# Performance work log

Hardware: AMD Instinct MI355X
Metric: run time of the kernel (lower is better)

Reference implementation:

```python
import jax, jax.numpy as jnp
import numpy as np

H = 16  # num_heads
EPS = 1e-6

def _sigma(t):
    # ELU(x)+1, the positive feature map used by Infini-attention linear memory
    return jax.nn.elu(t) + 1.0

def setup_inputs() -> dict:
    key = jax.random.key(0)
    ks = jax.random.split(key, 6)
    B, S, D = 1, 2048, 1024
    d = D // H
    std = 1.0 / np.sqrt(D)
    return {
        "x": jax.random.normal(ks[0], (B, S, D), dtype=jnp.float32),
        "M": jnp.zeros((H, d, d), dtype=jnp.float32),
        "z": jnp.zeros((H, d), dtype=jnp.float32),
        "Wq": jax.random.normal(ks[1], (D, D), dtype=jnp.float32) * std,
        "Wk": jax.random.normal(ks[2], (D, D), dtype=jnp.float32) * std,
        "Wv": jax.random.normal(ks[3], (D, D), dtype=jnp.float32) * std,
        "Wo": jax.random.normal(ks[4], (D, D), dtype=jnp.float32) * std,
        "beta": jnp.zeros((H,), dtype=jnp.float32),
    }

def reference(x, M, z, Wq, Wk, Wv, Wo, beta):
    B, S, D = x.shape
    d = D // H
    # projections -> [B, H, S, d]
    def proj(W):
        return (x @ W).reshape(B, S, H, d).transpose(0, 2, 1, 3)
    q, k, v = proj(Wq), proj(Wk), proj(Wv)

    # ---- local causal dot-product attention ----
    scale = 1.0 / jnp.sqrt(jnp.asarray(d, dtype=x.dtype))
    scores = jnp.einsum('bhqd,bhkd->bhqk', q, k) * scale  # [B,H,S,S]
    causal = jnp.tril(jnp.ones((S, S), dtype=bool))
    scores = jnp.where(causal, scores, jnp.asarray(-1e30, dtype=scores.dtype))
    A_dot = jnp.einsum('bhqk,bhkd->bhqd', jax.nn.softmax(scores, axis=-1), v)

    # ---- compressive memory retrieval (linear attention) ----
    sq = _sigma(q)                                       # [B,H,S,d]
    num = jnp.einsum('bhsd,hde->bhse', sq, M)            # [B,H,S,d]
    den = jnp.einsum('bhsd,hd->bhs', sq, z)[..., None]   # [B,H,S,1]
    A_mem = num / (den + EPS)

    # ---- learned gate blend ----
    g = jax.nn.sigmoid(beta).reshape(1, H, 1, 1)
    o = g * A_mem + (1.0 - g) * A_dot                    # [B,H,S,d]
    out = o.transpose(0, 2, 1, 3).reshape(B, S, D) @ Wo  # [B,S,D]

    # ---- memory update (stateful, no_grad in original) ----
    sk = _sigma(k)
    M_new = jax.lax.stop_gradient(M + jnp.einsum('bhsd,bhse->hde', sk, v))
    z_new = jax.lax.stop_gradient(z + sk.sum(axis=(0, 2)))
    return out, M_new, z_new
```

## Files before the change

kernel.cpp:

```cpp
#include <hip/hip_runtime.h>

#define S_LEN 2048
#define D_MODEL 1024
#define NH 16
#define DH 64

typedef __attribute__((ext_vector_type(8))) short bf16x8;
typedef __attribute__((ext_vector_type(4))) float f32x4;

__device__ __forceinline__ f32x4 mfma16(bf16x8 a, bf16x8 b, f32x4 c) {
  return __builtin_amdgcn_mfma_f32_16x16x32_bf16(a, b, c, 0, 0, 0);
}

__device__ __forceinline__ void ldst16(const ushort* g, ushort* l) {
  __builtin_amdgcn_global_load_lds(
      (const __attribute__((address_space(1))) void*)g,
      (__attribute__((address_space(3))) void*)l, 16, 0, 0);
}

__device__ __forceinline__ ushort bf16_rne(float f) {
  unsigned u = __float_as_uint(f);
  unsigned r = (u + 0x7FFFu + ((u >> 16) & 1u)) >> 16;
  return (ushort)r;
}
__device__ __forceinline__ float bf16_to_f(ushort u) {
  return __uint_as_float((unsigned)u << 16);
}

__global__ __launch_bounds__(256) void cast_bf16(
    const float* __restrict__ in, ushort* __restrict__ hi, int n4)
{
  int i = blockIdx.x * 256 + threadIdx.x;
  if (i >= n4) return;
  float4 v = ((const float4*)in)[i];
  ushort4 h;
  h.x = bf16_rne(v.x); h.y = bf16_rne(v.y);
  h.z = bf16_rne(v.z); h.w = bf16_rne(v.w);
  ((ushort4*)hi)[i] = h;
}

__global__ __launch_bounds__(256) void splitT(
    const float* __restrict__ W0, const float* __restrict__ W1,
    const float* __restrict__ W2, const float* __restrict__ W3,
    ushort* __restrict__ H0, ushort* __restrict__ L0,
    ushort* __restrict__ H1, ushort* __restrict__ L1,
    ushort* __restrict__ H2, ushort* __restrict__ L2,
    ushort* __restrict__ H3, ushort* __restrict__ L3)
{
  const int zz = blockIdx.z;
  const float* W = zz == 0 ? W0 : (zz == 1 ? W1 : (zz == 2 ? W2 : W3));
  ushort* H = zz == 0 ? H0 : (zz == 1 ? H1 : (zz == 2 ? H2 : H3));
  ushort* L = zz == 0 ? L0 : (zz == 1 ? L1 : (zz == 2 ? L2 : L3));
  __shared__ float ts[32][33];
  const int k0 = blockIdx.x * 32, n0 = blockIdx.y * 32;
  const int r = threadIdx.x >> 3, c4 = (threadIdx.x & 7) * 4;
  float4 v = *(const float4*)&W[(size_t)(k0 + r) * D_MODEL + n0 + c4];
  ts[r][c4 + 0] = v.x; ts[r][c4 + 1] = v.y; ts[r][c4 + 2] = v.z; ts[r][c4 + 3] = v.w;
  __syncthreads();
  ushort4 h, l;
#pragma unroll
  for (int ii = 0; ii < 4; ii++) {
    float f = ts[c4 + ii][r];
    ushort hb = bf16_rne(f);
    ushort lb = bf16_rne(f - __uint_as_float((unsigned)hb << 16));
    ((ushort*)&h)[ii] = hb;
    ((ushort*)&l)[ii] = lb;
  }
  *(ushort4*)&H[(size_t)(n0 + r) * D_MODEL + k0 + c4] = h;
  *(ushort4*)&L[(size_t)(n0 + r) * D_MODEL + k0 + c4] = l;
}

template<int TN>
__global__ __launch_bounds__(256, 3) void gemm_t(
    const ushort* __restrict__ Ah,
    const ushort* __restrict__ B0h, const ushort* __restrict__ B0l,
    const ushort* __restrict__ B1h, const ushort* __restrict__ B1l,
    const ushort* __restrict__ B2h, const ushort* __restrict__ B2l,
    float* __restrict__ C0, int K, int mode,
    ushort* __restrict__ aqb, ushort* __restrict__ akb,
    ushort* __restrict__ akbT, ushort* __restrict__ avbT)
{
  const int t = threadIdx.x;
  const int w = t >> 6, lane = t & 63;
  const int quad = lane >> 4, lr = lane & 15;
  const int bx = blockIdx.x;
  const int bw = (bx * TN) >> 10;
  const int n0 = (bx * TN) & 1023;
  const int m0 = blockIdx.y * 64;
  const ushort* Bh = bw == 0 ? B0h : (bw == 1 ? B1h : B2h);
  const ushort* Bl = bw == 0 ? B0l : (bw == 1 ? B1l : B2l);

  __shared__ ushort sAh[64 * 32], sBh[TN * 32], sBl[TN * 32];

  constexpr int NF = TN / 32;
  f32x4 acc[2][NF];
#pragma unroll
  for (int mi = 0; mi < 2; mi++)
#pragma unroll
    for (int ni = 0; ni < NF; ni++)
#pragma unroll
      for (int r = 0; r < 4; r++) acc[mi][ni][r] = 0.f;

  const int mbase = (w & 1) * 32;
  const int nbase = (w >> 1) * (TN / 2);
  const int rowA = w * 16 + (lane >> 2), kcA = (lane & 3) * 8;

  for (int k0 = 0; k0 < K; k0 += 32) {
    __syncthreads();
    ldst16(Ah + (size_t)(m0 + rowA) * K + k0 + kcA, &sAh[w * 512]);
#pragma unroll
    for (int i = 0; i < TN / 64; i++) {
      int rowB = w * (TN / 4) + i * 16 + (lane >> 2);
      int base = (w * (TN / 4) + i * 16) * 32;
      ldst16(Bh + (size_t)(n0 + rowB) * K + k0 + kcA, &sBh[base]);
      ldst16(Bl + (size_t)(n0 + rowB) * K + k0 + kcA, &sBl[base]);
    }
    __syncthreads();

    bf16x8 ah[2], bh[NF], bl[NF];
#pragma unroll
    for (int mi = 0; mi < 2; mi++)
      ah[mi] = *(const bf16x8*)&sAh[(mbase + mi * 16 + lr) * 32 + quad * 8];
#pragma unroll
    for (int ni = 0; ni < NF; ni++) {
      int rown = nbase + ni * 16 + lr;
      bh[ni] = *(const bf16x8*)&sBh[rown * 32 + quad * 8];
      bl[ni] = *(const bf16x8*)&sBl[rown * 32 + quad * 8];
    }
#pragma unroll
    for (int mi = 0; mi < 2; mi++)
#pragma unroll
      for (int ni = 0; ni < NF; ni++) {
        acc[mi][ni] = mfma16(ah[mi], bh[ni], acc[mi][ni]);
        acc[mi][ni] = mfma16(ah[mi], bl[ni], acc[mi][ni]);
      }
  }

  if (mode == 0) {
#pragma unroll
    for (int mi = 0; mi < 2; mi++)
#pragma unroll
      for (int ni = 0; ni < NF; ni++)
#pragma unroll
        for (int r = 0; r < 4; r++) {
          int row = m0 + mbase + mi * 16 + quad * 4 + r;
          int col = n0 + nbase + ni * 16 + lr;
          C0[(size_t)row * 1024 + col] = acc[mi][ni][r];
        }
  } else if (bw == 0) {
#pragma unroll
    for (int mi = 0; mi < 2; mi++)
#pragma unroll
      for (int ni = 0; ni < NF; ni++)
#pragma unroll
        for (int r = 0; r < 4; r++) {
          int row = m0 + mbase + mi * 16 + quad * 4 + r;
          int col = n0 + nbase + ni * 16 + lr;
          aqb[(size_t)row * 1024 + col] = bf16_rne(acc[mi][ni][r] * 0.125f);
        }
  } else if (bw == 1) {
#pragma unroll
    for (int mi = 0; mi < 2; mi++)
#pragma unroll
      for (int ni = 0; ni < NF; ni++) {
        int row0 = m0 + mbase + mi * 16 + quad * 4;
        int col = n0 + nbase + ni * 16 + lr;
        ushort4 pk;
#pragma unroll
        for (int r = 0; r < 4; r++) {
          ushort b = bf16_rne(acc[mi][ni][r]);
          ((ushort*)&pk)[r] = b;
          akb[(size_t)(row0 + r) * 1024 + col] = b;
        }
        *(ushort4*)&akbT[(size_t)col * 2048 + row0] = pk;
      }
  } else {
#pragma unroll
    for (int mi = 0; mi < 2; mi++)
#pragma unroll
      for (int ni = 0; ni < NF; ni++) {
        int row0 = m0 + mbase + mi * 16 + quad * 4;
        int col = n0 + nbase + ni * 16 + lr;
        ushort4 pk;
#pragma unroll
        for (int r = 0; r < 4; r++)
          ((ushort*)&pk)[r] = bf16_rne(acc[mi][ni][r]);
        *(ushort4*)&avbT[(size_t)col * 2048 + row0] = pk;
      }
  }
}

__global__ __launch_bounds__(256, 3) void attn_fused(
    const ushort* __restrict__ qb, const ushort* __restrict__ kb,
    const ushort* __restrict__ vbT, const ushort* __restrict__ kbT,
    const float* __restrict__ Mmem, const float* __restrict__ zmem,
    const float* __restrict__ beta,
    ushort* __restrict__ oh,
    float* __restrict__ Mout, float* __restrict__ zout)
{
  const int t = threadIdx.x;
  const int w = t >> 6, lane = t & 63;
  const int quad = lane >> 4, lr = lane & 15;

  __shared__ __align__(16) ushort sBuf[24576];
  __shared__ float drow[64];
  __shared__ float sL[64];

  if (blockIdx.x < 16) {
    const int h = blockIdx.x;
    float* red = (float*)sBuf;
    f32x4 acc[4][4];
#pragma unroll
    for (int mt = 0; mt < 4; mt++)
#pragma unroll
      for (int nt = 0; nt < 4; nt++)
#pragma unroll
        for (int r = 0; r < 4; r++) acc[mt][nt][r] = 0.f;
    float accZ[4] = {0.f, 0.f, 0.f, 0.f};

#pragma unroll 2
    for (int step = 0; step < 16; step++) {
      int k0 = w * 512 + step * 32;
      bf16x8 ah[4], al[4];
#pragma unroll
      for (int mt = 0; mt < 4; mt++) {
        bf16x8 raw = *(const bf16x8*)&kbT[(size_t)(h * 64 + mt * 16 + lr) * 2048 + k0 + quad * 8];
        bf16x8 hh, ll;
#pragma unroll
        for (int j = 0; j < 8; j++) {
          float f = bf16_to_f((ushort)raw[j]);
          float s = f > 0.f ? f + 1.f : __expf(f);
          accZ[mt] += s;
          ushort hb = bf16_rne(s);
          hh[j] = (short)hb;
          ll[j] = (short)bf16_rne(s - bf16_to_f(hb));
        }
        ah[mt] = hh; al[mt] = ll;
      }
      bf16x8 bv[4];
#pragma unroll
      for (int nt = 0; nt < 4; nt++)
        bv[nt] = *(const bf16x8*)&vbT[(size_t)(h * 64 + nt * 16 + lr) * 2048 + k0 + quad * 8];
#pragma unroll
      for (int mt = 0; mt < 4; mt++)
#pragma unroll
        for (int nt = 0; nt < 4; nt++) {
          acc[mt][nt] = mfma16(ah[mt], bv[nt], acc[mt][nt]);
          acc[mt][nt] = mfma16(al[mt], bv[nt], acc[mt][nt]);
        }
    }
#pragma unroll
    for (int mt = 0; mt < 4; mt++) {
      accZ[mt] += __shfl_xor(accZ[mt], 16);
      accZ[mt] += __shfl_xor(accZ[mt], 32);
    }
    if (w < 2) {
#pragma unroll
      for (int mt = 0; mt < 4; mt++)
#pragma unroll
        for (int nt = 0; nt < 4; nt++)
#pragma unroll
          for (int r = 0; r < 4; r++)
            red[w * 4096 + (mt * 16 + quad * 4 + r) * 64 + nt * 16 + lr] = acc[mt][nt][r];
    }
    __syncthreads();
    if (w >= 2) {
#pragma unroll
      for (int mt = 0; mt < 4; mt++)
#pragma unroll
        for (int nt = 0; nt < 4; nt++)
#pragma unroll
          for (int r = 0; r < 4; r++)
            red[(w - 2) * 4096 + (mt * 16 + quad * 4 + r) * 64 + nt * 16 + lr] += acc[mt][nt][r];
    }
    __syncthreads();
    for (int i = t; i < 4096; i += 256)
      Mout[(size_t)h * 4096 + i] = Mmem[(size_t)h * 4096 + i] + red[i] + red[4096 + i];
    __syncthreads();
    if (quad == 0) {
#pragma unroll
      for (int mt = 0; mt < 4; mt++)
        red[w * 64 + mt * 16 + lr] = accZ[mt];
    }
    __syncthreads();
    if (t < 64)
      zout[h * 64 + t] = zmem[h * 64 + t] + red[t] + red[64 + t] + red[128 + t] + red[192 + t];
    return;
  }

  const int a  = blockIdx.x - 16;
  const int h  = a >> 5;
  const int p  = (a >> 1) & 15;
  const int qt = (a & 1) ? p : 31 - p;
  const int s0 = qt * 64;
  const int ntiles = (qt + 2) >> 1;

  const int SPQ = 0, SK = 8192, SVT = 16384;

#pragma unroll
  for (int i = 0; i < 2; i++) {
    int li = w * 2 + i;
    int row = li * 8 + (lane >> 3);
    int cg = ((lane & 7) - row) & 7;
    ldst16(qb + (size_t)(s0 + row) * 1024 + h * 64 + cg * 8, &sBuf[SPQ + li * 512]);
  }
  __syncthreads();
  const int arow = w * 16 + lr;
  const bf16x8 aq0 = *(const bf16x8*)&sBuf[SPQ + arow * 64 + ((quad + arow) & 7) * 8];
  const bf16x8 aq1 = *(const bf16x8*)&sBuf[SPQ + arow * 64 + ((4 + quad + arow) & 7) * 8];

  f32x4 oacc[4];
#pragma unroll
  for (int ni = 0; ni < 4; ni++)
#pragma unroll
    for (int r = 0; r < 4; r++) oacc[ni][r] = 0.f;
  f32x4 lacc;
#pragma unroll
  for (int r = 0; r < 4; r++) lacc[r] = 0.f;
  bf16x8 bone;
#pragma unroll
  for (int j = 0; j < 8; j++) bone[j] = (lr == 0) ? (short)0x3F80 : (short)0;

  for (int jt = 0; jt < ntiles; jt++) {
    const int j0 = jt * 128;
    __syncthreads();
#pragma unroll
    for (int i = 0; i < 4; i++) {
      int li = w * 4 + i;
      int rowK = li * 8 + (lane >> 3);
      int cgK = ((lane & 7) - rowK) & 7;
      ldst16(kb + (size_t)(j0 + rowK) * 1024 + h * 64 + cgK * 8,
             &sBuf[SK + li * 512]);
      int rowV = li * 4 + (lane >> 4);
      int cgV = ((lane & 15) - rowV) & 15;
      ldst16(vbT + (size_t)(h * 64 + rowV) * 2048 + j0 + cgV * 8,
             &sBuf[SVT + li * 512]);
    }
    __syncthreads();

    f32x4 sc[8];
#pragma unroll
    for (int nj = 0; nj < 8; nj++) {
      int brow = nj * 16 + lr;
      bf16x8 b0 = *(const bf16x8*)&sBuf[SK + brow * 64 + ((quad + brow) & 7) * 8];
      bf16x8 b1 = *(const bf16x8*)&sBuf[SK + brow * 64 + ((4 + quad + brow) & 7) * 8];
      f32x4 z4; z4[0] = z4[1] = z4[2] = z4[3] = 0.f;
      z4 = mfma16(aq0, b0, z4);
      sc[nj] = mfma16(aq1, b1, z4);
    }
    if (jt == ntiles - 1) {
#pragma unroll
      for (int nj = 0; nj < 8; nj++)
#pragma unroll
        for (int r = 0; r < 4; r++)
          if (j0 + nj * 16 + lr > s0 + w * 16 + quad * 4 + r) sc[nj][r] = -1e30f;
    }

#pragma unroll
    for (int nj = 0; nj < 8; nj++)
#pragma unroll
      for (int r = 0; r < 4; r++) {
        float e = exp2f(fmaf(sc[nj][r], 1.4426950408889634f, -23.083120654223414f));
        int rr2 = w * 16 + quad * 4 + r;
        sBuf[SPQ + rr2 * 128 + ((nj * 16 + lr + rr2 * 8) & 127)] = bf16_rne(e);
      }

    bf16x8 ap[4];
#pragma unroll
    for (int kf = 0; kf < 4; kf++)
      ap[kf] = *(const bf16x8*)&sBuf[SPQ + arow * 128 + ((kf * 32 + quad * 8 + arow * 8) & 127)];
#pragma unroll
    for (int ni = 0; ni < 4; ni++) {
      int brow = ni * 16 + lr;
#pragma unroll
      for (int kf = 0; kf < 4; kf++) {
        bf16x8 bv = *(const bf16x8*)&sBuf[SVT + brow * 128 + ((kf * 32 + quad * 8 + brow * 8) & 127)];
        oacc[ni] = mfma16(ap[kf], bv, oacc[ni]);
      }
    }
#pragma unroll
    for (int kf = 0; kf < 4; kf++)
      lacc = mfma16(ap[kf], bone, lacc);
  }
  __syncthreads();

  float* sF  = (float*)sBuf;
  float* sO  = sF;
  float* ssq = sF + 4352;
  if (lr == 0) {
#pragma unroll
    for (int r = 0; r < 4; r++) sL[w * 16 + quad * 4 + r] = lacc[r];
  }
#pragma unroll
  for (int ni = 0; ni < 4; ni++)
#pragma unroll
    for (int r = 0; r < 4; r++)
      sO[(w * 16 + quad * 4 + r) * 68 + ni * 16 + lr] = oacc[ni][r];

#pragma unroll
  for (int i = 0; i < 4; i++) {
    int idx4 = t + i * 256;
    int r = idx4 >> 4, c4 = (idx4 & 15) * 4;
    ushort4 u4 = *(const ushort4*)&qb[(size_t)(s0 + r) * 1024 + h * 64 + c4];
#pragma unroll
    for (int j = 0; j < 4; j++) {
      float qv = bf16_to_f(((const ushort*)&u4)[j]) * 8.0f;
      ssq[(c4 + j) * 68 + r] = qv > 0.f ? qv + 1.f : __expf(qv);
    }
  }
  __syncthreads();

  {
    int rr2 = t >> 2, part = t & 3;
    float ds = 0.f;
#pragma unroll
    for (int jj = 0; jj < 16; jj++) {
      int c = part + jj * 4;
      ds = fmaf(ssq[c * 68 + rr2], zmem[h * 64 + c], ds);
    }
    ds += __shfl_xor(ds, 1);
    ds += __shfl_xor(ds, 2);
    if (part == 0) drow[rr2] = ds + 1e-6f;
  }
  __syncthreads();

  const int tx = t & 15, ty = t >> 4;
  float nacc[4][4] = {};
#pragma unroll 8
  for (int dd = 0; dd < 64; dd++) {
    float4 av = *(const float4*)&ssq[dd * 68 + ty * 4];
    float4 bv = *(const float4*)&Mmem[(size_t)h * 4096 + dd * 64 + tx * 4];
    float aa[4] = {av.x, av.y, av.z, av.w};
    float bb[4] = {bv.x, bv.y, bv.z, bv.w};
#pragma unroll
    for (int i = 0; i < 4; i++)
#pragma unroll
      for (int j = 0; j < 4; j++)
        nacc[i][j] = fmaf(aa[i], bb[j], nacc[i][j]);
  }
  float g = 1.f / (1.f + __expf(-beta[h]));
#pragma unroll
  for (int i = 0; i < 4; i++) {
    int r = ty * 4 + i;
    float invd = 1.f / drow[r];
    float invl = (1.f - g) / sL[r];
    float4 od = *(const float4*)&sO[r * 68 + tx * 4];
    float b0 = g * nacc[i][0] * invd + od.x * invl;
    float b1 = g * nacc[i][1] * invd + od.y * invl;
    float b2 = g * nacc[i][2] * invd + od.z * invl;
    float b3 = g * nacc[i][3] * invd + od.w * invl;
    ushort4 hh;
    hh.x = bf16_rne(b0); hh.y = bf16_rne(b1);
    hh.z = bf16_rne(b2); hh.w = bf16_rne(b3);
    *(ushort4*)&oh[(size_t)(s0 + r) * 1024 + h * 64 + tx * 4] = hh;
  }
}

extern "C" void kernel_launch(void* const* d_in, const int* in_sizes, int n_in,
                              void* d_out, int out_size, void* d_ws, size_t ws_size,
                              hipStream_t stream) {
  const float* x    = (const float*)d_in[0];
  const float* M    = (const float*)d_in[1];
  const float* z    = (const float*)d_in[2];
  const float* Wq   = (const float*)d_in[3];
  const float* Wk   = (const float*)d_in[4];
  const float* Wv   = (const float*)d_in[5];
  const float* Wo   = (const float*)d_in[6];
  const float* beta = (const float*)d_in[7];

  float* out  = (float*)d_out;
  float* Mout = out + (size_t)S_LEN * D_MODEL;
  float* zout = Mout + NH*DH*DH;

  const size_t NE = (size_t)S_LEN * D_MODEL;
  const size_t WE = (size_t)D_MODEL * D_MODEL;
  ushort* xh  = (ushort*)d_ws;
  ushort* wqh = xh + NE;
  ushort* wql = wqh + WE;
  ushort* wkh = wql + WE;
  ushort* wkl = wkh + WE;
  ushort* wvh = wkl + WE;
  ushort* wvl = wvh + WE;
  ushort* woh = wvl + WE;
  ushort* wol = woh + WE;
  ushort* qb  = wol + WE;
  ushort* kb  = qb + NE;
  ushort* kbT = kb + NE;
  ushort* vbT = kbT + NE;
  ushort* ohb = vbT + NE;

  cast_bf16<<<dim3(NE/4/256), 256, 0, stream>>>(x, xh, (int)(NE/4));
  splitT<<<dim3(32, 32, 4), 256, 0, stream>>>(Wq, Wk, Wv, Wo,
      wqh, wql, wkh, wkl, wvh, wvl, woh, wol);

  gemm_t<128><<<dim3(24, 32), 256, 0, stream>>>(xh,
      wqh, wql, wkh, wkl, wvh, wvl,
      (float*)nullptr, D_MODEL, 1, qb, kb, kbT, vbT);

  attn_fused<<<dim3(528), 256, 0, stream>>>(qb, kb, vbT, kbT,
      M, z, beta, ohb, Mout, zout);

  gemm_t<64><<<dim3(16, 32), 256, 0, stream>>>(ohb,
      woh, wol, woh, wol, woh, wol,
      out, D_MODEL, 0, nullptr, nullptr, nullptr, nullptr);
}
```

Measured before the change: 196.6 us.

## Double attention block to 512 threads, splitting key tiles across wave halves

The fused attention kernel now launches 512 threads per block. In the attention path each group of four waves handles half of each 128-key tile, and the two partial O and L accumulators are combined through shared memory. In the memory-update path eight waves split the sequence and reduce in stages. The aim is more waves in flight per block to hide latency, at the cost of extra LDS reductions, more barriers, and possibly more register pressure under the new launch bounds.

```diff
diff --git a/kernel.cpp b/kernel.cpp
--- a/kernel.cpp
+++ b/kernel.cpp
@@ -190,7 +190,7 @@
   }
 }
 
-__global__ __launch_bounds__(256, 3) void attn_fused(
+__global__ __launch_bounds__(512, 4) void attn_fused(
     const ushort* __restrict__ qb, const ushort* __restrict__ kb,
     const ushort* __restrict__ vbT, const ushort* __restrict__ kbT,
     const float* __restrict__ Mmem, const float* __restrict__ zmem,
@@ -219,8 +219,8 @@
     float accZ[4] = {0.f, 0.f, 0.f, 0.f};
 
 #pragma unroll 2
-    for (int step = 0; step < 16; step++) {
-      int k0 = w * 512 + step * 32;
+    for (int step = 0; step < 8; step++) {
+      int k0 = w * 256 + step * 32;
       bf16x8 ah[4], al[4];
 #pragma unroll
       for (int mt = 0; mt < 4; mt++) {
@@ -264,17 +264,20 @@
             red[w * 4096 + (mt * 16 + quad * 4 + r) * 64 + nt * 16 + lr] = acc[mt][nt][r];
     }
     __syncthreads();
-    if (w >= 2) {
-#pragma unroll
-      for (int mt = 0; mt < 4; mt++)
-#pragma unroll
-        for (int nt = 0; nt < 4; nt++)
-#pragma unroll
-          for (int r = 0; r < 4; r++)
-            red[(w - 2) * 4096 + (mt * 16 + quad * 4 + r) * 64 + nt * 16 + lr] += acc[mt][nt][r];
-    }
-    __syncthreads();
-    for (int i = t; i < 4096; i += 256)
+#pragma unroll
+    for (int grp = 1; grp < 4; grp++) {
+      if ((w >> 1) == grp) {
+#pragma unroll
+        for (int mt = 0; mt < 4; mt++)
+#pragma unroll
+          for (int nt = 0; nt < 4; nt++)
+#pragma unroll
+            for (int r = 0; r < 4; r++)
+              red[(w & 1) * 4096 + (mt * 16 + quad * 4 + r) * 64 + nt * 16 + lr] += acc[mt][nt][r];
+      }
+      __syncthreads();
+    }
+    for (int i = t; i < 4096; i += 512)
       Mout[(size_t)h * 4096 + i] = Mmem[(size_t)h * 4096 + i] + red[i] + red[4096 + i];
     __syncthreads();
     if (quad == 0) {
@@ -283,8 +286,12 @@
         red[w * 64 + mt * 16 + lr] = accZ[mt];
     }
     __syncthreads();
-    if (t < 64)
-      zout[h * 64 + t] = zmem[h * 64 + t] + red[t] + red[64 + t] + red[128 + t] + red[192 + t];
+    if (t < 64) {
+      float s = 0.f;
+#pragma unroll
+      for (int ww = 0; ww < 8; ww++) s += red[ww * 64 + t];
+      zout[h * 64 + t] = zmem[h * 64 + t] + s;
+    }
     return;
   }
 
@@ -294,18 +301,17 @@
   const int qt = (a & 1) ? p : 31 - p;
   const int s0 = qt * 64;
   const int ntiles = (qt + 2) >> 1;
+  const int wq = w & 3, jh = w >> 2;
 
   const int SPQ = 0, SK = 8192, SVT = 16384;
 
-#pragma unroll
-  for (int i = 0; i < 2; i++) {
-    int li = w * 2 + i;
-    int row = li * 8 + (lane >> 3);
+  {
+    int row = w * 8 + (lane >> 3);
     int cg = ((lane & 7) - row) & 7;
-    ldst16(qb + (size_t)(s0 + row) * 1024 + h * 64 + cg * 8, &sBuf[SPQ + li * 512]);
+    ldst16(qb + (size_t)(s0 + row) * 1024 + h * 64 + cg * 8, &sBuf[SPQ + w * 512]);
   }
   __syncthreads();
-  const int arow = w * 16 + lr;
+  const int arow = wq * 16 + lr;
   const bf16x8 aq0 = *(const bf16x8*)&sBuf[SPQ + arow * 64 + ((quad + arow) & 7) * 8];
   const bf16x8 aq1 = *(const bf16x8*)&sBuf[SPQ + arow * 64 + ((4 + quad + arow) & 7) * 8];
 
@@ -327,79 +333,96 @@
 #pragma unroll
     for (int i = 0; i < 4; i++) {
       int li = w * 4 + i;
-      int rowK = li * 8 + (lane >> 3);
-      int cgK = ((lane & 7) - rowK) & 7;
-      ldst16(kb + (size_t)(j0 + rowK) * 1024 + h * 64 + cgK * 8,
-             &sBuf[SK + li * 512]);
-      int rowV = li * 4 + (lane >> 4);
-      int cgV = ((lane & 15) - rowV) & 15;
-      ldst16(vbT + (size_t)(h * 64 + rowV) * 2048 + j0 + cgV * 8,
-             &sBuf[SVT + li * 512]);
-    }
-    __syncthreads();
-
-    f32x4 sc[8];
-#pragma unroll
-    for (int nj = 0; nj < 8; nj++) {
-      int brow = nj * 16 + lr;
+      if (li < 16) {
+        int rowK = li * 8 + (lane >> 3);
+        int cgK = ((lane & 7) - rowK) & 7;
+        ldst16(kb + (size_t)(j0 + rowK) * 1024 + h * 64 + cgK * 8,
+               &sBuf[SK + li * 512]);
+      } else {
+        int lv = li - 16;
+        int rowV = lv * 4 + (lane >> 4);
+        int cgV = ((lane & 15) - rowV) & 15;
+        ldst16(vbT + (size_t)(h * 64 + rowV) * 2048 + j0 + cgV * 8,
+               &sBuf[SVT + lv * 512]);
+      }
+    }
+    __syncthreads();
+
+    f32x4 sc[4];
+#pragma unroll
+    for (int nj = 0; nj < 4; nj++) {
+      int njg = jh * 4 + nj;
+      int brow = njg * 16 + lr;
       bf16x8 b0 = *(const bf16x8*)&sBuf[SK + brow * 64 + ((quad + brow) & 7) * 8];
       bf16x8 b1 = *(const bf16x8*)&sBuf[SK + brow * 64 + ((4 + quad + brow) & 7) * 8];
       f32x4 z4; z4[0] = z4[1] = z4[2] = z4[3] = 0.f;
-      z4 = mfma16(aq0, b0, z4);
-      sc[nj] = mfma16(aq1, b1, z4);
+      z4 = mfma16(b0, aq0, z4);
+      sc[nj] = mfma16(b1, aq1, z4);
     }
     if (jt == ntiles - 1) {
 #pragma unroll
-      for (int nj = 0; nj < 8; nj++)
+      for (int nj = 0; nj < 4; nj++)
 #pragma unroll
         for (int r = 0; r < 4; r++)
-          if (j0 + nj * 16 + lr > s0 + w * 16 + quad * 4 + r) sc[nj][r] = -1e30f;
-    }
-
-#pragma unroll
-    for (int nj = 0; nj < 8; nj++)
+          if (j0 + (jh * 4 + nj) * 16 + quad * 4 + r > s0 + arow) sc[nj][r] = -1e30f;
+    }
+
+#pragma unroll
+    for (int nj = 0; nj < 4; nj++) {
+      ushort4 pk;
 #pragma unroll
       for (int r = 0; r < 4; r++) {
         float e = exp2f(fmaf(sc[nj][r], 1.4426950408889634f, -23.083120654223414f));
-        int rr2 = w * 16 + quad * 4 + r;
-        sBuf[SPQ + rr2 * 128 + ((nj * 16 + lr + rr2 * 8) & 127)] = bf16_rne(e);
-      }
-
-    bf16x8 ap[4];
-#pragma unroll
-    for (int kf = 0; kf < 4; kf++)
-      ap[kf] = *(const bf16x8*)&sBuf[SPQ + arow * 128 + ((kf * 32 + quad * 8 + arow * 8) & 127)];
-#pragma unroll
-    for (int ni = 0; ni < 4; ni++) {
-      int brow = ni * 16 + lr;
-#pragma unroll
-      for (int kf = 0; kf < 4; kf++) {
+        ((ushort*)&pk)[r] = bf16_rne(e);
+      }
+      int col = (jh * 4 + nj) * 16 + quad * 4;
+      *(ushort4*)&sBuf[SPQ + arow * 128 + ((col + arow * 8) & 127)] = pk;
+    }
+
+#pragma unroll
+    for (int kfi = 0; kfi < 2; kfi++) {
+      int kf = jh * 2 + kfi;
+      bf16x8 ap = *(const bf16x8*)&sBuf[SPQ + arow * 128 + ((kf * 32 + quad * 8 + arow * 8) & 127)];
+#pragma unroll
+      for (int ni = 0; ni < 4; ni++) {
+        int brow = ni * 16 + lr;
         bf16x8 bv = *(const bf16x8*)&sBuf[SVT + brow * 128 + ((kf * 32 + quad * 8 + brow * 8) & 127)];
-        oacc[ni] = mfma16(ap[kf], bv, oacc[ni]);
-      }
-    }
-#pragma unroll
-    for (int kf = 0; kf < 4; kf++)
-      lacc = mfma16(ap[kf], bone, lacc);
+        oacc[ni] = mfma16(ap, bv, oacc[ni]);
+      }
+      lacc = mfma16(ap, bone, lacc);
+    }
   }
   __syncthreads();
 
   float* sF  = (float*)sBuf;
   float* sO  = sF;
   float* ssq = sF + 4352;
-  if (lr == 0) {
-#pragma unroll
-    for (int r = 0; r < 4; r++) sL[w * 16 + quad * 4 + r] = lacc[r];
-  }
-#pragma unroll
-  for (int ni = 0; ni < 4; ni++)
-#pragma unroll
-    for (int r = 0; r < 4; r++)
-      sO[(w * 16 + quad * 4 + r) * 68 + ni * 16 + lr] = oacc[ni][r];
-
-#pragma unroll
-  for (int i = 0; i < 4; i++) {
-    int idx4 = t + i * 256;
+  if (jh == 0) {
+#pragma unroll
+    for (int ni = 0; ni < 4; ni++)
+#pragma unroll
+      for (int r = 0; r < 4; r++)
+        sO[(wq * 16 + quad * 4 + r) * 68 + ni * 16 + lr] = oacc[ni][r];
+    if (lr == 0) {
+#pragma unroll
+      for (int r = 0; r < 4; r++) sL[wq * 16 + quad * 4 + r] = lacc[r];
+    }
+  }
+  __syncthreads();
+  if (jh == 1) {
+#pragma unroll
+    for (int ni = 0; ni < 4; ni++)
+#pragma unroll
+      for (int r = 0; r < 4; r++)
+        sO[(wq * 16 + quad * 4 + r) * 68 + ni * 16 + lr] += oacc[ni][r];
+    if (lr == 0) {
+#pragma unroll
+      for (int r = 0; r < 4; r++) sL[wq * 16 + quad * 4 + r] += lacc[r];
+    }
+  }
+#pragma unroll
+  for (int i = 0; i < 2; i++) {
+    int idx4 = t + i * 512;
     int r = idx4 >> 4, c4 = (idx4 & 15) * 4;
     ushort4 u4 = *(const ushort4*)&qb[(size_t)(s0 + r) * 1024 + h * 64 + c4];
 #pragma unroll
@@ -411,44 +434,43 @@
   __syncthreads();
 
   {
-    int rr2 = t >> 2, part = t & 3;
+    int rr2 = t >> 3, part = t & 7;
     float ds = 0.f;
 #pragma unroll
-    for (int jj = 0; jj < 16; jj++) {
-      int c = part + jj * 4;
+    for (int jj = 0; jj < 8; jj++) {
+      int c = part + jj * 8;
       ds = fmaf(ssq[c * 68 + rr2], zmem[h * 64 + c], ds);
     }
     ds += __shfl_xor(ds, 1);
     ds += __shfl_xor(ds, 2);
+    ds += __shfl_xor(ds, 4);
     if (part == 0) drow[rr2] = ds + 1e-6f;
   }
   __syncthreads();
 
-  const int tx = t & 15, ty = t >> 4;
-  float nacc[4][4] = {};
+  const int tx = t & 15, ty2 = t >> 4;
+  float nacc[2][4] = {};
 #pragma unroll 8
   for (int dd = 0; dd < 64; dd++) {
-    float4 av = *(const float4*)&ssq[dd * 68 + ty * 4];
+    float a0 = ssq[dd * 68 + ty2 * 2 + 0];
+    float a1 = ssq[dd * 68 + ty2 * 2 + 1];
     float4 bv = *(const float4*)&Mmem[(size_t)h * 4096 + dd * 64 + tx * 4];
-    float aa[4] = {av.x, av.y, av.z, av.w};
-    float bb[4] = {bv.x, bv.y, bv.z, bv.w};
-#pragma unroll
-    for (int i = 0; i < 4; i++)
-#pragma unroll
-      for (int j = 0; j < 4; j++)
-        nacc[i][j] = fmaf(aa[i], bb[j], nacc[i][j]);
+    nacc[0][0] = fmaf(a0, bv.x, nacc[0][0]); nacc[0][1] = fmaf(a0, bv.y, nacc[0][1]);
+    nacc[0][2] = fmaf(a0, bv.z, nacc[0][2]); nacc[0][3] = fmaf(a0, bv.w, nacc[0][3]);
+    nacc[1][0] = fmaf(a1, bv.x, nacc[1][0]); nacc[1][1] = fmaf(a1, bv.y, nacc[1][1]);
+    nacc[1][2] = fmaf(a1, bv.z, nacc[1][2]); nacc[1][3] = fmaf(a1, bv.w, nacc[1][3]);
   }
   float g = 1.f / (1.f + __expf(-beta[h]));
 #pragma unroll
-  for (int i = 0; i < 4; i++) {
-    int r = ty * 4 + i;
-    float invd = 1.f / drow[r];
+  for (int i = 0; i < 2; i++) {
+    int r = ty2 * 2 + i;
+    float invd = g / drow[r];
     float invl = (1.f - g) / sL[r];
     float4 od = *(const float4*)&sO[r * 68 + tx * 4];
-    float b0 = g * nacc[i][0] * invd + od.x * invl;
-    float b1 = g * nacc[i][1] * invd + od.y * invl;
-    float b2 = g * nacc[i][2] * invd + od.z * invl;
-    float b3 = g * nacc[i][3] * invd + od.w * invl;
+    float b0 = nacc[i][0] * invd + od.x * invl;
+    float b1 = nacc[i][1] * invd + od.y * invl;
+    float b2 = nacc[i][2] * invd + od.z * invl;
+    float b3 = nacc[i][3] * invd + od.w * invl;
     ushort4 hh;
     hh.x = bf16_rne(b0); hh.y = bf16_rne(b1);
     hh.z = bf16_rne(b2); hh.w = bf16_rne(b3);
@@ -497,7 +519,7 @@
       wqh, wql, wkh, wkl, wvh, wvl,
       (float*)nullptr, D_MODEL, 1, qb, kb, kbT, vbT);
 
-  attn_fused<<<dim3(528), 256, 0, stream>>>(qb, kb, vbT, kbT,
+  attn_fused<<<dim3(528), 512, 0, stream>>>(qb, kb, vbT, kbT,
       M, z, beta, ohb, Mout, zout);
 
   gemm_t<64><<<dim3(16, 32), 256, 0, stream>>>(ohb,
```

New measurement: 209.6 us. 1.07x slower.

## Read K and V fragments directly from global memory instead of staging through LDS

Applied to the files above, without the earlier changes.

The attention loop no longer stages Q, K and V tiles into shared memory with barriers. MFMA operands are now loaded straight from global memory, and the QK^T product is computed transposed so each lane's probabilities pack into ushort4 writes to LDS. Dropping the staging shrinks shared memory, which allows raising the occupancy hint from 3 to 4 blocks. The cost is redundant, less coalesced global/L2 traffic in place of LDS reuse across waves.

```diff
diff --git a/kernel.cpp b/kernel.cpp
--- a/kernel.cpp
+++ b/kernel.cpp
@@ -190,7 +190,7 @@
   }
 }
 
-__global__ __launch_bounds__(256, 3) void attn_fused(
+__global__ __launch_bounds__(256, 4) void attn_fused(
     const ushort* __restrict__ qb, const ushort* __restrict__ kb,
     const ushort* __restrict__ vbT, const ushort* __restrict__ kbT,
     const float* __restrict__ Mmem, const float* __restrict__ zmem,
@@ -202,7 +202,7 @@
   const int w = t >> 6, lane = t & 63;
   const int quad = lane >> 4, lr = lane & 15;
 
-  __shared__ __align__(16) ushort sBuf[24576];
+  __shared__ __align__(16) ushort sBuf[17408];
   __shared__ float drow[64];
   __shared__ float sL[64];
 
@@ -295,19 +295,9 @@
   const int s0 = qt * 64;
   const int ntiles = (qt + 2) >> 1;
 
-  const int SPQ = 0, SK = 8192, SVT = 16384;
-
-#pragma unroll
-  for (int i = 0; i < 2; i++) {
-    int li = w * 2 + i;
-    int row = li * 8 + (lane >> 3);
-    int cg = ((lane & 7) - row) & 7;
-    ldst16(qb + (size_t)(s0 + row) * 1024 + h * 64 + cg * 8, &sBuf[SPQ + li * 512]);
-  }
-  __syncthreads();
   const int arow = w * 16 + lr;
-  const bf16x8 aq0 = *(const bf16x8*)&sBuf[SPQ + arow * 64 + ((quad + arow) & 7) * 8];
-  const bf16x8 aq1 = *(const bf16x8*)&sBuf[SPQ + arow * 64 + ((4 + quad + arow) & 7) * 8];
+  const bf16x8 aq0 = *(const bf16x8*)&qb[(size_t)(s0 + arow) * 1024 + h * 64 + quad * 8];
+  const bf16x8 aq1 = *(const bf16x8*)&qb[(size_t)(s0 + arow) * 1024 + h * 64 + 32 + quad * 8];
 
   f32x4 oacc[4];
 #pragma unroll
@@ -321,66 +311,52 @@
 #pragma unroll
   for (int j = 0; j < 8; j++) bone[j] = (lr == 0) ? (short)0x3F80 : (short)0;
 
+  const ushort* kbh  = kb  + h * 64;
+  const ushort* vbh  = vbT + (size_t)(h * 64) * 2048;
+
   for (int jt = 0; jt < ntiles; jt++) {
     const int j0 = jt * 128;
-    __syncthreads();
-#pragma unroll
-    for (int i = 0; i < 4; i++) {
-      int li = w * 4 + i;
-      int rowK = li * 8 + (lane >> 3);
-      int cgK = ((lane & 7) - rowK) & 7;
-      ldst16(kb + (size_t)(j0 + rowK) * 1024 + h * 64 + cgK * 8,
-             &sBuf[SK + li * 512]);
-      int rowV = li * 4 + (lane >> 4);
-      int cgV = ((lane & 15) - rowV) & 15;
-      ldst16(vbT + (size_t)(h * 64 + rowV) * 2048 + j0 + cgV * 8,
-             &sBuf[SVT + li * 512]);
-    }
-    __syncthreads();
 
     f32x4 sc[8];
 #pragma unroll
     for (int nj = 0; nj < 8; nj++) {
-      int brow = nj * 16 + lr;
-      bf16x8 b0 = *(const bf16x8*)&sBuf[SK + brow * 64 + ((quad + brow) & 7) * 8];
-      bf16x8 b1 = *(const bf16x8*)&sBuf[SK + brow * 64 + ((4 + quad + brow) & 7) * 8];
+      const ushort* kr = kbh + (size_t)(j0 + nj * 16 + lr) * 1024;
+      bf16x8 k0 = *(const bf16x8*)&kr[quad * 8];
+      bf16x8 k1 = *(const bf16x8*)&kr[32 + quad * 8];
       f32x4 z4; z4[0] = z4[1] = z4[2] = z4[3] = 0.f;
-      z4 = mfma16(aq0, b0, z4);
-      sc[nj] = mfma16(aq1, b1, z4);
+      z4 = mfma16(k0, aq0, z4);
+      sc[nj] = mfma16(k1, aq1, z4);
     }
     if (jt == ntiles - 1) {
 #pragma unroll
       for (int nj = 0; nj < 8; nj++)
 #pragma unroll
         for (int r = 0; r < 4; r++)
-          if (j0 + nj * 16 + lr > s0 + w * 16 + quad * 4 + r) sc[nj][r] = -1e30f;
-    }
-
-#pragma unroll
-    for (int nj = 0; nj < 8; nj++)
+          if (j0 + nj * 16 + quad * 4 + r > s0 + arow) sc[nj][r] = -1e30f;
+    }
+
+#pragma unroll
+    for (int nj = 0; nj < 8; nj++) {
+      ushort4 pk;
 #pragma unroll
       for (int r = 0; r < 4; r++) {
         float e = exp2f(fmaf(sc[nj][r], 1.4426950408889634f, -23.083120654223414f));
-        int rr2 = w * 16 + quad * 4 + r;
-        sBuf[SPQ + rr2 * 128 + ((nj * 16 + lr + rr2 * 8) & 127)] = bf16_rne(e);
-      }
-
-    bf16x8 ap[4];
-#pragma unroll
-    for (int kf = 0; kf < 4; kf++)
-      ap[kf] = *(const bf16x8*)&sBuf[SPQ + arow * 128 + ((kf * 32 + quad * 8 + arow * 8) & 127)];
-#pragma unroll
-    for (int ni = 0; ni < 4; ni++) {
-      int brow = ni * 16 + lr;
-#pragma unroll
-      for (int kf = 0; kf < 4; kf++) {
-        bf16x8 bv = *(const bf16x8*)&sBuf[SVT + brow * 128 + ((kf * 32 + quad * 8 + brow * 8) & 127)];
-        oacc[ni] = mfma16(ap[kf], bv, oacc[ni]);
-      }
-    }
-#pragma unroll
-    for (int kf = 0; kf < 4; kf++)
-      lacc = mfma16(ap[kf], bone, lacc);
+        ((ushort*)&pk)[r] = bf16_rne(e);
+      }
+      int col = nj * 16 + quad * 4;
+      *(ushort4*)&sBuf[arow * 128 + ((col + arow * 8) & 127)] = pk;
+    }
+
+#pragma unroll
+    for (int kf = 0; kf < 4; kf++) {
+      bf16x8 ap = *(const bf16x8*)&sBuf[arow * 128 + ((kf * 32 + quad * 8 + arow * 8) & 127)];
+#pragma unroll
+      for (int ni = 0; ni < 4; ni++) {
+        bf16x8 bv = *(const bf16x8*)&vbh[(size_t)(ni * 16 + lr) * 2048 + j0 + kf * 32 + quad * 8];
+        oacc[ni] = mfma16(ap, bv, oacc[ni]);
+      }
+      lacc = mfma16(ap, bone, lacc);
+    }
   }
   __syncthreads();
 
@@ -442,13 +418,13 @@
 #pragma unroll
   for (int i = 0; i < 4; i++) {
     int r = ty * 4 + i;
-    float invd = 1.f / drow[r];
+    float invd = g / drow[r];
     float invl = (1.f - g) / sL[r];
     float4 od = *(const float4*)&sO[r * 68 + tx * 4];
-    float b0 = g * nacc[i][0] * invd + od.x * invl;
-    float b1 = g * nacc[i][1] * invd + od.y * invl;
-    float b2 = g * nacc[i][2] * invd + od.z * invl;
-    float b3 = g * nacc[i][3] * invd + od.w * invl;
+    float b0 = nacc[i][0] * invd + od.x * invl;
+    float b1 = nacc[i][1] * invd + od.y * invl;
+    float b2 = nacc[i][2] * invd + od.z * invl;
+    float b3 = nacc[i][3] * invd + od.w * invl;
     ushort4 hh;
     hh.x = bf16_rne(b0); hh.y = bf16_rne(b1);
     hh.z = bf16_rne(b2); hh.w = bf16_rne(b3);
```

Result: slower. 283.8 us (+44.3%).
